# Kernel optimization log

Hardware: AMD Instinct MI355X
Metric: run time of the kernel (lower is better)

## Reference

```python
import jax, jax.numpy as jnp
import numpy as np

B, N, E, H, T, FC = 16, 4096, 131072, 16, 3, 20


def setup_inputs() -> dict:
    key = jax.random.key(0)
    ks = jax.random.split(key, 16)
    F = jnp.eye(3, dtype=jnp.float32)[None] + 0.05 * jax.random.normal(ks[0], (B, 3, 3), dtype=jnp.float32)
    node_pos = jax.random.uniform(ks[1], (N, 3), dtype=jnp.float32)
    edge_src = jax.random.randint(ks[2], (E,), 0, N)
    edge_dst = jax.random.randint(ks[3], (E,), 0, N)
    edge_type = jax.random.randint(ks[4], (E,), 0, T)
    sc = lambda k, s: jax.random.normal(k, s, dtype=jnp.float32) / np.float32(np.sqrt(s[0]))
    return {
        'F': F, 'node_pos': node_pos,
        'edge_src': edge_src, 'edge_dst': edge_dst, 'edge_type': edge_type,
        'W_in': sc(ks[5], (3, H)),
        'fc1_0': sc(ks[6], (T, FC)), 'fc2_0': sc(ks[7], (FC, 1)), 'W_0': sc(ks[8], (H, H)),
        'fc1_1': sc(ks[9], (T, FC)), 'fc2_1': sc(ks[10], (FC, 1)), 'W_1': sc(ks[11], (H, H)),
        'W_out': sc(ks[12], (H, 3)),
        'w': jax.random.uniform(ks[13], (N * N,), dtype=jnp.float32),
    }


def _message_passing(Fx, edge_src, edge_dst, edge_oh,
                     W_in, fc1_0, fc2_0, W_0, fc1_1, fc2_1, W_1, W_out):
    # simplified stand-in for e3nn MessagePassing_v1: per-edge scalar gate from
    # edge-type MLP (fc_neurons=[3,20]), gather-scatter aggregation / sqrt(deg)
    inv_sqrt_deg = np.float32(1.0 / np.sqrt(edge_src.shape[0] / Fx.shape[1]))
    h = Fx @ W_in  # [B,N,H]
    for fc1, fc2, Wl in ((fc1_0, fc2_0, W_0), (fc1_1, fc2_1, W_1)):
        ew = jax.nn.relu(edge_oh @ fc1) @ fc2          # [E,1]
        msg = h[:, edge_src] * ew[None]                # [B,E,H]
        agg = jnp.zeros_like(h).at[:, edge_dst].add(msg) * inv_sqrt_deg
        h = jax.nn.relu(agg @ Wl)
    return h @ W_out  # [B,N,3]


def reference(F, node_pos, edge_src, edge_dst, edge_type,
              W_in, fc1_0, fc2_0, W_0, fc1_1, fc2_1, W_1, W_out, w):
    edge_oh = jax.nn.one_hot(edge_type, T, dtype=F.dtype)
    Fx = jnp.einsum('bij,nj->bni', F, node_pos)                     # deform positions
    h = _message_passing(Fx, edge_src, edge_dst, edge_oh,
                         W_in, fc1_0, fc2_0, W_0, fc1_1, fc2_1, W_1, W_out)
    Fx_ij = h[:, edge_src] - h[:, edge_dst]                         # [B,E,3]
    x_ij = jnp.einsum('bij,bej->bei', jnp.linalg.inv(F), Fx_ij)     # [B,E,3]
    n = node_pos.shape[0]
    a = Fx_ij[:, :n]  # original loop indexes first N edges with node index i
    c = x_ij[:, :n]
    W2 = w.reshape(n, n)
    # vectorized form of: sum_ij w[i*n+j] * kron(Fx_ij[b,i], x_ij[b,j])
    t = jnp.einsum('ij,bip->bjp', W2, a)                            # [B,N,3]
    stress = jnp.einsum('bjp,bjq->bpq', t, c).reshape(F.shape[0], 9)
    return stress
```

## Files before the change

### kernel.cpp

```cpp
#include <hip/hip_runtime.h>

#define N_NODES 4096
#define N_EDGES 131072
#define BATCH   16
#define HDIM    16
#define FCDIM   20
#define BH      256
#define ISD     0.17677669529663687f
#define NBSTRESS 1024

__device__ __forceinline__ float f4get(const float4& v, int k) {
    return k == 0 ? v.x : (k == 1 ? v.y : (k == 2 ? v.z : v.w));
}

template<int CTRL, int RM>
__device__ __forceinline__ float dpp_add(float v) {
    int sh = __builtin_amdgcn_update_dpp(0, __float_as_int(v), CTRL, RM, 0xF, true);
    return v + __int_as_float(sh);
}
__device__ __forceinline__ float wave_sum64(float v) {
    v = dpp_add<0xB1, 0xF>(v);
    v = dpp_add<0x4E, 0xF>(v);
    v = dpp_add<0x141,0xF>(v);
    v = dpp_add<0x140,0xF>(v);
    v = dpp_add<0x142,0xA>(v);
    v = dpp_add<0x143,0xC>(v);
    return v;
}

__global__ void setup_kernel(const float* __restrict__ F, const float* __restrict__ W_in,
                             const float* __restrict__ fc1_0, const float* __restrict__ fc2_0,
                             const float* __restrict__ fc1_1, const float* __restrict__ fc2_1,
                             float* __restrict__ ew, float* __restrict__ G,
                             float* __restrict__ invF, float* __restrict__ out144,
                             int* __restrict__ cnt) {
    int t = threadIdx.x;
    if (t < 6) {
        const float* fc1 = (t < 3) ? fc1_0 : fc1_1;
        const float* fc2 = (t < 3) ? fc2_0 : fc2_1;
        int ty = t % 3;
        float s = 0.f;
        for (int f = 0; f < FCDIM; ++f) {
            float v = fc1[ty * FCDIM + f];
            v = v > 0.f ? v : 0.f;
            s += v * fc2[f];
        }
        ew[t] = s;
    }
    for (int idx = t; idx < BATCH * 3 * HDIM; idx += 256) {
        int b = idx / 48, r = idx % 48, j = r / HDIM, k = r % HDIM;
        float s = 0.f;
        for (int i = 0; i < 3; ++i) s += F[b * 9 + i * 3 + j] * W_in[i * HDIM + k];
        G[idx] = s;
    }
    if (t < BATCH) {
        const float* f = F + t * 9;
        float a00=f[0],a01=f[1],a02=f[2],a10=f[3],a11=f[4],a12=f[5],a20=f[6],a21=f[7],a22=f[8];
        float det = a00*(a11*a22-a12*a21) - a01*(a10*a22-a12*a20) + a02*(a10*a21-a11*a20);
        float id = 1.f/det;
        float* o = invF + t*9;
        o[0]=(a11*a22-a12*a21)*id; o[1]=(a02*a21-a01*a22)*id; o[2]=(a01*a12-a02*a11)*id;
        o[3]=(a12*a20-a10*a22)*id; o[4]=(a00*a22-a02*a20)*id; o[5]=(a02*a10-a00*a12)*id;
        o[6]=(a10*a21-a11*a20)*id; o[7]=(a01*a20-a00*a21)*id; o[8]=(a00*a11-a01*a10)*id;
    }
    if (t < 144) out144[t] = 0.f;
    for (int i = t; i < N_NODES; i += 256) cnt[i] = 0;
}

__global__ void h0_hist_kernel(const float* __restrict__ pos, const float* __restrict__ G,
                               float* __restrict__ h0,
                               const int* __restrict__ edst, int* __restrict__ cnt) {
    int bid = blockIdx.x;
    int t = threadIdx.x;
    if (bid < 1024) {
        int id = bid * 256 + t;
        int n  = id >> 6;
        int c4 = (id & 63) << 2;
        int b  = c4 >> 4;
        int k  = c4 & 15;
        float p0 = pos[n*3+0], p1 = pos[n*3+1], p2 = pos[n*3+2];
        const float* g = G + b*48 + k;
        float4 r;
        r.x = p0*g[0] + p1*g[16] + p2*g[32];
        r.y = p0*g[1] + p1*g[17] + p2*g[33];
        r.z = p0*g[2] + p1*g[18] + p2*g[34];
        r.w = p0*g[3] + p1*g[19] + p2*g[35];
        *(float4*)(h0 + n*BH + c4) = r;
    } else {
        int e = (bid - 1024) * 256 + t;
        if (e < N_EDGES) atomicAdd(&cnt[edst[e]], 1);
    }
}

__global__ void scan_kernel(const int* __restrict__ cnt, int* __restrict__ off,
                            int* __restrict__ cursor) {
    __shared__ int wsum[4];
    int t = threadIdx.x;
    int lane = t & 63, wave = t >> 6;
    int base = t * 16;
    int loc[16];
    int s = 0;
    #pragma unroll
    for (int i = 0; i < 16; ++i) { loc[i] = s; s += cnt[base + i]; }
    int pre = s;
    #pragma unroll
    for (int o = 1; o < 64; o <<= 1) {
        int v = __shfl_up(pre, o);
        if (lane >= o) pre += v;
    }
    if (lane == 63) wsum[wave] = pre;
    __syncthreads();
    int woff = 0;
    #pragma unroll
    for (int w = 0; w < 4; ++w) if (w < wave) woff += wsum[w];
    int excl = woff + pre - s;
    #pragma unroll
    for (int i = 0; i < 16; ++i) {
        int v = excl + loc[i];
        off[base + i] = v;
        cursor[base + i] = v;
    }
    if (t == 255) off[N_NODES] = excl + s;
}
__global__ void fill_kernel(const int* __restrict__ src, const int* __restrict__ dst,
                            const int* __restrict__ typ, int* __restrict__ cursor,
                            int* __restrict__ sedge) {
    int e = blockIdx.x * 256 + threadIdx.x;
    if (e < N_EDGES) {
        int p = atomicAdd(&cursor[dst[e]], 1);
        sedge[p] = src[e] | (typ[e] << 16);
    }
}

__global__ void layer_kernel(const float* __restrict__ h_in, float* __restrict__ h_out,
                             const int* __restrict__ off, const int* __restrict__ sedge,
                             const float* __restrict__ ew3, const float* __restrict__ W) {
    __shared__ float Wl[256];
    __shared__ float aggS[2][16*17 + 4];
    int t = threadIdx.x;
    Wl[t] = W[t];
    int wave = t >> 6, lane = t & 63;
    int node = wave >> 1;
    int half = wave & 1;
    int d = blockIdx.x * 2 + node;
    float e0 = ew3[0], e1 = ew3[1], e2 = ew3[2];
    int beg = off[d], end = off[d+1];
    int col = half * 128 + lane * 2;
    float2 acc = {0.f, 0.f};
    int it = beg;
    for (; it + 7 < end; it += 8) {
        int v[8]; float2 hv[8];
        #pragma unroll
        for (int u = 0; u < 8; ++u) v[u] = sedge[it + u];
        #pragma unroll
        for (int u = 0; u < 8; ++u)
            hv[u] = *(const float2*)(h_in + (v[u] & 0xFFFF) * BH + col);
        #pragma unroll
        for (int u = 0; u < 8; ++u) {
            int ty = v[u] >> 16;
            float wg = (ty == 0) ? e0 : (ty == 1 ? e1 : e2);
            acc.x += wg * hv[u].x; acc.y += wg * hv[u].y;
        }
    }
    for (; it < end; ++it) {
        int v = sedge[it];
        int ty = v >> 16;
        float wg = (ty == 0) ? e0 : (ty == 1 ? e1 : e2);
        float2 hv = *(const float2*)(h_in + (v & 0xFFFF) * BH + col);
        acc.x += wg * hv.x; acc.y += wg * hv.y;
    }
    int b = col >> 4, k0 = col & 15;
    aggS[node][b*17 + k0]     = acc.x * ISD;
    aggS[node][b*17 + k0 + 1] = acc.y * ISD;
    __syncthreads();
    int en = t >> 7, c2 = (t & 127) * 2;
    int eb = c2 >> 4, ek = c2 & 15;
    const float* arow = aggS[en] + eb * 17;
    float o0 = 0.f, o1 = 0.f;
    #pragma unroll
    for (int k = 0; k < 16; ++k) {
        float av = arow[k];
        o0 += av * Wl[k*16 + ek];
        o1 += av * Wl[k*16 + ek + 1];
    }
    int ed = blockIdx.x * 2 + en;
    float2 r;
    r.x = o0 > 0.f ? o0 : 0.f;
    r.y = o1 > 0.f ? o1 : 0.f;
    *(float2*)(h_out + ed*BH + c2) = r;
}

__global__ void ac_kernel(const float* __restrict__ h2, const float* __restrict__ Wout,
                          const int* __restrict__ esrc, const int* __restrict__ edst,
                          const float* __restrict__ invF,
                          float* __restrict__ a, float* __restrict__ c) {
    __shared__ float iF[144];
    __shared__ float Wo[48];
    int t = threadIdx.x;
    if (t < 144) iF[t] = invF[t];
    else if (t < 192) Wo[t - 144] = Wout[t - 144];
    __syncthreads();
    int id = blockIdx.x * 256 + t;
    int i = id >> 4, b = id & 15;
    int s = esrc[i], d = edst[i];
    const float* hs = h2 + s*BH + b*HDIM;
    const float* hd = h2 + d*BH + b*HDIM;
    float a0 = 0.f, a1 = 0.f, a2 = 0.f;
    #pragma unroll
    for (int k = 0; k < 16; ++k) {
        float dv = hs[k] - hd[k];
        a0 += dv*Wo[k*3+0]; a1 += dv*Wo[k*3+1]; a2 += dv*Wo[k*3+2];
    }
    float* ap = a + i*48 + b*3;
    ap[0]=a0; ap[1]=a1; ap[2]=a2;
    const float* m = iF + b*9;
    float* cp = c + i*48 + b*3;
    cp[0] = m[0]*a0 + m[1]*a1 + m[2]*a2;
    cp[1] = m[3]*a0 + m[4]*a1 + m[5]*a2;
    cp[2] = m[6]*a0 + m[7]*a1 + m[8]*a2;
}

__global__ __launch_bounds__(256, 4)
void stress_fused_kernel(const float* __restrict__ W2, const float* __restrict__ a,
                         const float* __restrict__ c, float* __restrict__ P) {
    int t = threadIdx.x;
    int lane = t & 63;
    int wave = t >> 6;
    int cg   = __builtin_amdgcn_readfirstlane(wave * 12);
    int jb    = (blockIdx.x & 15) * 256;
    int strip = blockIdx.x >> 4;
    int i0    = strip * 64;
    int j = jb + lane * 4;
    const float* w2p = W2 + (size_t)i0 * N_NODES + j;
    const float* ap  = a + (size_t)i0 * 48 + cg;
    float4 acc[4][3];
    #pragma unroll
    for (int jj = 0; jj < 4; ++jj)
        #pragma unroll
        for (int q = 0; q < 3; ++q) acc[jj][q] = make_float4(0.f,0.f,0.f,0.f);
    float4 w[4];
    #pragma unroll
    for (int u = 0; u < 4; ++u)
        w[u] = *(const float4*)(w2p + (size_t)u * N_NODES);
    #pragma unroll 1
    for (int base = 0; base < 64; base += 4) {
        float4 wn[4];
        #pragma unroll
        for (int u = 0; u < 4; ++u) {
            int r = base + 4 + u; if (r > 63) r = 63;
            wn[u] = *(const float4*)(w2p + (size_t)r * N_NODES);
        }
        #pragma unroll
        for (int u = 0; u < 4; ++u) {
            const float* ar = ap + (size_t)(base + u) * 48;
            float4 x = *(const float4*)(ar);
            float4 y = *(const float4*)(ar + 4);
            float4 z = *(const float4*)(ar + 8);
            #pragma unroll
            for (int jj = 0; jj < 4; ++jj) {
                float wv = f4get(w[u], jj);
                acc[jj][0].x += wv*x.x; acc[jj][0].y += wv*x.y;
                acc[jj][0].z += wv*x.z; acc[jj][0].w += wv*x.w;
                acc[jj][1].x += wv*y.x; acc[jj][1].y += wv*y.y;
                acc[jj][1].z += wv*y.z; acc[jj][1].w += wv*y.w;
                acc[jj][2].x += wv*z.x; acc[jj][2].y += wv*z.y;
                acc[jj][2].z += wv*z.z; acc[jj][2].w += wv*z.w;
            }
        }
        #pragma unroll
        for (int u = 0; u < 4; ++u) w[u] = wn[u];
    }
    float s[36];
    #pragma unroll
    for (int m = 0; m < 36; ++m) s[m] = 0.f;
    #pragma unroll
    for (int jj = 0; jj < 4; ++jj) {
        const float* cvp = c + (size_t)(jb + lane * 4 + jj) * 48 + cg;
        float4 c0 = *(const float4*)(cvp);
        float4 c1 = *(const float4*)(cvp + 4);
        float4 c2 = *(const float4*)(cvp + 8);
        float cv[12] = {c0.x,c0.y,c0.z,c0.w, c1.x,c1.y,c1.z,c1.w, c2.x,c2.y,c2.z,c2.w};
        #pragma unroll
        for (int cc = 0; cc < 12; ++cc) {
            float tv = f4get(acc[jj][cc >> 2], cc & 3);
            int qb = (cc / 3) * 3;
            s[cc*3+0] += tv * cv[qb+0];
            s[cc*3+1] += tv * cv[qb+1];
            s[cc*3+2] += tv * cv[qb+2];
        }
    }
    #pragma unroll
    for (int m = 0; m < 36; ++m) s[m] = wave_sum64(s[m]);
    if (lane == 63) {
        #pragma unroll
        for (int m = 0; m < 36; ++m) {
            int cc = m / 3, q = m % 3;
            int bp = cg + cc;
            P[(size_t)((bp / 3) * 9 + (bp % 3) * 3 + q) * NBSTRESS + blockIdx.x] = s[m];
        }
    }
}

__global__ void stress_reduce_kernel(const float* __restrict__ P, float* __restrict__ out) {
    __shared__ float wsum[4];
    int t = threadIdx.x, lane = t & 63, wave = t >> 6;
    const float* p = P + (size_t)blockIdx.x * NBSTRESS;
    float4 v = *(const float4*)(p + t * 4);
    float s = v.x + v.y + v.z + v.w;
    #pragma unroll
    for (int o = 1; o < 64; o <<= 1) s += __shfl_xor(s, o);
    if (lane == 0) wsum[wave] = s;
    __syncthreads();
    if (t == 0) out[blockIdx.x] = wsum[0] + wsum[1] + wsum[2] + wsum[3];
}

extern "C" void kernel_launch(void* const* d_in, const int* in_sizes, int n_in,
                              void* d_out, int out_size, void* d_ws, size_t ws_size,
                              hipStream_t stream) {
    const float* F     = (const float*)d_in[0];
    const float* pos   = (const float*)d_in[1];
    const int*   esrc  = (const int*)d_in[2];
    const int*   edst  = (const int*)d_in[3];
    const int*   etyp  = (const int*)d_in[4];
    const float* W_in  = (const float*)d_in[5];
    const float* fc1_0 = (const float*)d_in[6];
    const float* fc2_0 = (const float*)d_in[7];
    const float* W_0   = (const float*)d_in[8];
    const float* fc1_1 = (const float*)d_in[9];
    const float* fc2_1 = (const float*)d_in[10];
    const float* W_1   = (const float*)d_in[11];
    const float* W_out = (const float*)d_in[12];
    const float* w2    = (const float*)d_in[13];
    float* out = (float*)d_out;

    float* ws   = (float*)d_ws;
    float* ew   = ws;
    float* G    = ws + 16;
    float* invF = ws + 800;
    float* bufA = ws + 1024;
    float* bufB = bufA + N_NODES*BH;
    float* aArr = bufB + N_NODES*BH;
    float* cArr = aArr + N_NODES*48;
    int* cnt    = (int*)(cArr + N_NODES*48);
    int* off    = cnt + N_NODES;
    int* cursor = off + N_NODES + 1;
    int* sedge  = cursor + N_NODES;
    float* P    = (float*)(sedge + N_EDGES);

    setup_kernel<<<1, 256, 0, stream>>>(F, W_in, fc1_0, fc2_0, fc1_1, fc2_1, ew, G, invF, out, cnt);
    h0_hist_kernel<<<1536, 256, 0, stream>>>(pos, G, bufA, edst, cnt);
    scan_kernel<<<1, 256, 0, stream>>>(cnt, off, cursor);
    fill_kernel<<<512, 256, 0, stream>>>(esrc, edst, etyp, cursor, sedge);
    layer_kernel<<<2048, 256, 0, stream>>>(bufA, bufB, off, sedge, ew,     W_0);
    layer_kernel<<<2048, 256, 0, stream>>>(bufB, bufA, off, sedge, ew + 3, W_1);
    ac_kernel<<<256, 256, 0, stream>>>(bufA, W_out, esrc, edst, invF, aArr, cArr);
    stress_fused_kernel<<<NBSTRESS, 256, 0, stream>>>(w2, aArr, cArr, P);
    stress_reduce_kernel<<<144, 256, 0, stream>>>(P, out);
}
```

Measured before the change: 223.0 us.

## Widen stress kernel j-tile to 8 columns and stage a rows in LDS

Each thread of the stress kernel now computes 8 output columns instead of 4, halving the number of blocks and doubling register accumulators. The strip's a rows are staged once into shared memory instead of being read from global per wave. This raises arithmetic per W2/a load and cuts redundant a traffic. In exchange occupancy drops (launch bounds 4 to 2) and register pressure rises, and the partial buffer and reduce kernel are resized to match.

```diff
diff --git a/kernel.cpp b/kernel.cpp
--- a/kernel.cpp
+++ b/kernel.cpp
@@ -7,7 +7,7 @@
 #define FCDIM   20
 #define BH      256
 #define ISD     0.17677669529663687f
-#define NBSTRESS 1024
+#define NBSTRESS 512
 
 __device__ __forceinline__ float f4get(const float4& v, int k) {
     return k == 0 ? v.x : (k == 1 ? v.y : (k == 2 ? v.z : v.w));
@@ -220,45 +220,55 @@
     cp[2] = m[6]*a0 + m[7]*a1 + m[8]*a2;
 }
 
-__global__ __launch_bounds__(256, 4)
+__global__ __launch_bounds__(256, 2)
 void stress_fused_kernel(const float* __restrict__ W2, const float* __restrict__ a,
                          const float* __restrict__ c, float* __restrict__ P) {
+    __shared__ float sa[64 * 48];
     int t = threadIdx.x;
     int lane = t & 63;
     int wave = t >> 6;
-    int cg   = __builtin_amdgcn_readfirstlane(wave * 12);
-    int jb    = (blockIdx.x & 15) * 256;
-    int strip = blockIdx.x >> 4;
+    int cg   = wave * 12;
+    int jb    = (blockIdx.x & 7) * 512;
+    int strip = blockIdx.x >> 3;
     int i0    = strip * 64;
-    int j = jb + lane * 4;
+    {
+        const float4* ga = (const float4*)(a + (size_t)i0 * 48);
+        float4* la = (float4*)sa;
+        #pragma unroll
+        for (int k = 0; k < 3; ++k) la[t + k * 256] = ga[t + k * 256];
+    }
+    __syncthreads();
+    int j = jb + lane * 8;
     const float* w2p = W2 + (size_t)i0 * N_NODES + j;
-    const float* ap  = a + (size_t)i0 * 48 + cg;
-    float4 acc[4][3];
-    #pragma unroll
-    for (int jj = 0; jj < 4; ++jj)
+    float4 acc[8][3];
+    #pragma unroll
+    for (int jj = 0; jj < 8; ++jj)
         #pragma unroll
         for (int q = 0; q < 3; ++q) acc[jj][q] = make_float4(0.f,0.f,0.f,0.f);
-    float4 w[4];
-    #pragma unroll
-    for (int u = 0; u < 4; ++u)
-        w[u] = *(const float4*)(w2p + (size_t)u * N_NODES);
+    float4 w[4][2];
+    #pragma unroll
+    for (int u = 0; u < 4; ++u) {
+        w[u][0] = *(const float4*)(w2p + (size_t)u * N_NODES);
+        w[u][1] = *(const float4*)(w2p + (size_t)u * N_NODES + 4);
+    }
     #pragma unroll 1
     for (int base = 0; base < 64; base += 4) {
-        float4 wn[4];
+        float4 wn[4][2];
         #pragma unroll
         for (int u = 0; u < 4; ++u) {
             int r = base + 4 + u; if (r > 63) r = 63;
-            wn[u] = *(const float4*)(w2p + (size_t)r * N_NODES);
+            wn[u][0] = *(const float4*)(w2p + (size_t)r * N_NODES);
+            wn[u][1] = *(const float4*)(w2p + (size_t)r * N_NODES + 4);
         }
         #pragma unroll
         for (int u = 0; u < 4; ++u) {
-            const float* ar = ap + (size_t)(base + u) * 48;
+            const float* ar = &sa[(base + u) * 48 + cg];
             float4 x = *(const float4*)(ar);
             float4 y = *(const float4*)(ar + 4);
             float4 z = *(const float4*)(ar + 8);
             #pragma unroll
-            for (int jj = 0; jj < 4; ++jj) {
-                float wv = f4get(w[u], jj);
+            for (int jj = 0; jj < 8; ++jj) {
+                float wv = f4get(w[u][jj >> 2], jj & 3);
                 acc[jj][0].x += wv*x.x; acc[jj][0].y += wv*x.y;
                 acc[jj][0].z += wv*x.z; acc[jj][0].w += wv*x.w;
                 acc[jj][1].x += wv*y.x; acc[jj][1].y += wv*y.y;
@@ -268,14 +278,14 @@
             }
         }
         #pragma unroll
-        for (int u = 0; u < 4; ++u) w[u] = wn[u];
+        for (int u = 0; u < 4; ++u) { w[u][0] = wn[u][0]; w[u][1] = wn[u][1]; }
     }
     float s[36];
     #pragma unroll
     for (int m = 0; m < 36; ++m) s[m] = 0.f;
     #pragma unroll
-    for (int jj = 0; jj < 4; ++jj) {
-        const float* cvp = c + (size_t)(jb + lane * 4 + jj) * 48 + cg;
+    for (int jj = 0; jj < 8; ++jj) {
+        const float* cvp = c + (size_t)(jb + lane * 8 + jj) * 48 + cg;
         float4 c0 = *(const float4*)(cvp);
         float4 c1 = *(const float4*)(cvp + 4);
         float4 c2 = *(const float4*)(cvp + 8);
@@ -305,8 +315,8 @@
     __shared__ float wsum[4];
     int t = threadIdx.x, lane = t & 63, wave = t >> 6;
     const float* p = P + (size_t)blockIdx.x * NBSTRESS;
-    float4 v = *(const float4*)(p + t * 4);
-    float s = v.x + v.y + v.z + v.w;
+    float2 v = *(const float2*)(p + t * 2);
+    float s = v.x + v.y;
     #pragma unroll
     for (int o = 1; o < 64; o <<= 1) s += __shfl_xor(s, o);
     if (lane == 0) wsum[wave] = s;
```

After: 267.1 us. 19.8% more time.
